# Kernel optimization log

Measured on AMD Instinct MI355X. Metric: run time of the kernel, lower is better.

## Reference

```python
import jax, jax.numpy as jnp
import numpy as np

DIM = 1024
HEADS = 16


def setup_inputs() -> dict:
    key = jax.random.key(0)
    ks = jax.random.split(key, 5)
    x = jax.random.normal(ks[0], (2, 2048, DIM), dtype=jnp.float32)
    # nn.Linear init-like scaling
    qkv_w = jax.random.normal(ks[1], (3 * DIM, DIM), dtype=jnp.float32) * (1.0 / np.sqrt(DIM))
    qkv_b = jax.random.normal(ks[2], (3 * DIM,), dtype=jnp.float32) * 0.02
    proj_w = jax.random.normal(ks[3], (DIM, DIM), dtype=jnp.float32) * (1.0 / np.sqrt(DIM))
    proj_b = jax.random.normal(ks[4], (DIM,), dtype=jnp.float32) * 0.02
    return {"x": x, "qkv_w": qkv_w, "qkv_b": qkv_b, "proj_w": proj_w, "proj_b": proj_b}


def reference(x, qkv_w, qkv_b, proj_w, proj_b):
    B, N, C = x.shape
    H = HEADS
    Dh = C // H
    scale = Dh ** -0.5
    # qkv: [B, N, 3C] -> [3, B, H, N, Dh]
    qkv = (x @ qkv_w.T + qkv_b).reshape(B, N, 3, H, Dh).transpose(2, 0, 3, 1, 4)
    q, k, v = qkv[0], qkv[1], qkv[2]
    attn = jnp.einsum('bhnd,bhmd->bhnm', q, k) * scale
    attn = jax.nn.softmax(attn, axis=-1)
    out = jnp.einsum('bhnm,bhmd->bhnd', attn, v)  # [B, H, N, Dh]
    out = out.transpose(0, 2, 1, 3).reshape(B, N, C)
    return out @ proj_w.T + proj_b
```

## Files before the change

### kernel.cpp

```cpp
#include <hip/hip_runtime.h>
#include <stdint.h>

#define DIM    1024
#define NHEADS 16
#define DH     64
#define SEQ    2048
#define BATCH  2
#define BHEADS (BATCH * NHEADS)
#define MROWS  (BATCH * SEQ)
#define SL2E   0.18033688011112042f

typedef __attribute__((ext_vector_type(8))) short bf16x8;
typedef __attribute__((ext_vector_type(4))) float f32x4;
typedef __attribute__((ext_vector_type(16))) float f32x16;
typedef unsigned short ushort_t;

#define GLDS(gp, lp) __builtin_amdgcn_global_load_lds( \
    (__attribute__((address_space(1))) void*)(gp), \
    (__attribute__((address_space(3))) void*)(lp), 16, 0, 0)

__device__ inline ushort_t f2bf(float f) {
    unsigned u = __builtin_bit_cast(unsigned, f);
    u += 0x7FFFu + ((u >> 16) & 1u);
    return (ushort_t)(u >> 16);
}

__global__ __launch_bounds__(256) void cvt_kernel(
    const float* __restrict__ s0, const float* __restrict__ s1, const float* __restrict__ s2,
    ushort_t* __restrict__ d0, ushort_t* __restrict__ d1, ushort_t* __restrict__ d2)
{
    const int N0 = MROWS * DIM;
    const int N1 = 3 * DIM * DIM;
    const int N2 = DIM * DIM;
    int e = (blockIdx.x * 256 + threadIdx.x) << 2;
    const float* src; ushort_t* dst;
    if (e < N0)                { src = s0 + e;             dst = d0 + e; }
    else if (e < N0 + N1)      { src = s1 + (e - N0);      dst = d1 + (e - N0); }
    else if (e < N0 + N1 + N2) { src = s2 + (e - N0 - N1); dst = d2 + (e - N0 - N1); }
    else return;
    float4 f = *(const float4*)src;
    ushort4 o;
    o.x = f2bf(f.x); o.y = f2bf(f.y); o.z = f2bf(f.z); o.w = f2bf(f.w);
    *(ushort4*)dst = o;
}

__global__ __launch_bounds__(512, 4) void qkv_gemm(
    const ushort_t* __restrict__ A, const ushort_t* __restrict__ W,
    const float* __restrict__ bias,
    ushort_t* __restrict__ Qw, ushort_t* __restrict__ Kw, ushort_t* __restrict__ Vt)
{
    __shared__ union {
        ushort_t stage[2][2][128 * 64];
        ushort_t T[128 * 136];
    } sm;

    const int tid  = threadIdx.x;
    const int lane = tid & 63;
    const int wave = tid >> 6;
    const int quad = lane >> 4;
    const int l16  = lane & 15;
    const int wm   = (wave >> 1) * 32;
    const int wn   = (wave & 1) * 64;
    const int bm   = blockIdx.x * 128;
    const int bn   = blockIdx.y * 128;
    const int Rl   = lane >> 3;
    const int pp   = lane & 7;

    f32x4 acc[2][4];
    for (int i = 0; i < 2; i++)
        for (int j = 0; j < 4; j++)
            for (int r = 0; r < 4; r++) acc[i][j][r] = 0.f;

    for (int j = 0; j < 2; j++) {
        int Rb = j * 64 + wave * 8;
        int R  = Rb + Rl;
        int c  = pp ^ (R & 7);
        GLDS(A + (size_t)(bm + R) * DIM + c * 8, sm.stage[0][0] + Rb * 64 + lane * 8);
        GLDS(W + (size_t)(bn + R) * DIM + c * 8, sm.stage[0][1] + Rb * 64 + lane * 8);
    }

    const int NT = DIM / 64;
    for (int t = 0; t < NT; t++) {
        if (t < NT - 1) {
            int kk = (t + 1) * 64;
            ushort_t* As1 = sm.stage[(t + 1) & 1][0];
            ushort_t* Bs1 = sm.stage[(t + 1) & 1][1];
            for (int j = 0; j < 2; j++) {
                int Rb = j * 64 + wave * 8;
                int R  = Rb + Rl;
                int c  = pp ^ (R & 7);
                GLDS(A + (size_t)(bm + R) * DIM + kk + c * 8, As1 + Rb * 64 + lane * 8);
                GLDS(W + (size_t)(bn + R) * DIM + kk + c * 8, Bs1 + Rb * 64 + lane * 8);
            }
            __asm volatile("s_waitcnt vmcnt(4)" ::: "memory");
        } else {
            __asm volatile("s_waitcnt vmcnt(0)" ::: "memory");
        }
        __asm volatile("s_barrier" ::: "memory");

        const ushort_t* Asb = sm.stage[t & 1][0];
        const ushort_t* Bsb = sm.stage[t & 1][1];
        for (int kh = 0; kh < 2; kh++) {
            bf16x8 a[2], b[4];
            for (int mi = 0; mi < 2; mi++) {
                int r = wm + mi * 16 + l16;
                a[mi] = *(const bf16x8*)(Asb + r * 64 + (((kh * 4 + quad) ^ (r & 7)) << 3));
            }
            for (int ni = 0; ni < 4; ni++) {
                int r = wn + ni * 16 + l16;
                b[ni] = *(const bf16x8*)(Bsb + r * 64 + (((kh * 4 + quad) ^ (r & 7)) << 3));
            }
            for (int mi = 0; mi < 2; mi++)
                for (int ni = 0; ni < 4; ni++)
                    acc[mi][ni] = __builtin_amdgcn_mfma_f32_16x16x32_bf16(a[mi], b[ni], acc[mi][ni], 0, 0, 0);
        }
        __asm volatile("s_waitcnt lgkmcnt(0)" ::: "memory");
        __asm volatile("s_barrier" ::: "memory");
    }

    const int three = bn >> 10;
    const float scale = (three == 0) ? SL2E : 1.0f;
    for (int ni = 0; ni < 4; ni++) {
        int cl   = wn + ni * 16 + l16;
        float bv = bias[bn + cl];
        for (int mi = 0; mi < 2; mi++)
            for (int reg = 0; reg < 4; reg++) {
                int r = wm + mi * 16 + quad * 4 + reg;
                sm.T[r * 136 + cl] = f2bf((acc[mi][ni][reg] + bv) * scale);
            }
    }
    __syncthreads();

    const int b = bm >> 11, npos0 = bm & 2047;
    if (three < 2) {
        int item = tid >> 1, sub = tid & 1;
        int r = item >> 1, hh = item & 1;
        int hc = (bn + hh * 64) & 1023;
        int h  = hc >> 6;
        ushort_t* dst = (three == 0 ? Qw : Kw) + ((size_t)(b * NHEADS + h) * SEQ + npos0 + r) * DH;
        const ushort_t* srcp = sm.T + r * 136 + hh * 64;
        for (int s = sub * 4; s < sub * 4 + 4; s++)
            *(uint4*)(dst + s * 8) = *(const uint4*)(srcp + s * 8);
    } else {
        int c = tid & 127, hh = (tid >> 7) & 1, sub = tid >> 8;
        int hc = (bn + c) & 1023;
        int h  = hc >> 6, d = hc & 63;
        ushort_t* dst = Vt + ((size_t)(b * NHEADS + h) * DH + d) * SEQ + npos0 + hh * 64;
        for (int s = sub * 4; s < sub * 4 + 4; s++) {
            union { ushort_t u[8]; uint4 v; } tmp;
            for (int k2 = 0; k2 < 8; k2++) {
                int o  = hh * 64 + s * 8 + k2;
                int po = (o & ~12) | ((o & 4) << 1) | ((o & 8) >> 1);
                tmp.u[k2] = sm.T[po * 136 + c];
            }
            *(uint4*)(dst + s * 8) = tmp.v;
        }
    }
}

__global__ __launch_bounds__(512, 4) void attn_kernel(
    const ushort_t* __restrict__ Qw, const ushort_t* __restrict__ Kw,
    const ushort_t* __restrict__ Vt, ushort_t* __restrict__ Ao)
{
    __shared__ union {
        ushort_t u[24576];
        float Lb[128][66];
    } sh;

    const int tid  = threadIdx.x;
    const int lane = tid & 63;
    const int wave = tid >> 6;
    const int grp  = wave >> 2;
    const int wg   = wave & 3;
    const int hi   = lane >> 5;
    const int l32  = lane & 31;
    const int Rl   = lane >> 3;
    const int pp   = lane & 7;

    const int bid  = blockIdx.x + 16 * blockIdx.y;
    const int bid2 = (bid & 7) * 64 + (bid >> 3);
    const int bh   = bid2 >> 4;
    const int q0   = (bid2 & 15) * 128;

    const ushort_t* Qh = Qw + (size_t)bh * SEQ * DH;
    const ushort_t* Kh = Kw + (size_t)bh * SEQ * DH;
    const ushort_t* Vh = Vt + (size_t)bh * DH * SEQ;

    ushort_t* const Qs = sh.u + 16384;

    for (int j = 0; j < 2; j++) {
        int Rb = j * 64 + wave * 8;
        int R  = Rb + Rl;
        int c  = pp ^ (R & 7);
        GLDS(Qh + (size_t)(q0 + R) * DH + c * 8, Qs + Rb * 64 + lane * 8);
    }
    for (int t = 0; t < 2; t++) {
        int R = wg * 8 + Rl;
        int c = pp ^ (R & 7);
        GLDS(Kh + (size_t)(t * 64 + grp * 32 + R) * DH + c * 8,
             sh.u + (t << 13) + grp * 2048 + wg * 512 + lane * 8);
        int Rd = wave * 8 + Rl;
        int cv = pp ^ (Rd & 7);
        GLDS(Vh + (size_t)Rd * SEQ + t * 64 + cv * 8,
             sh.u + (t << 13) + 4096 + wave * 512 + lane * 8);
    }
    __asm volatile("s_waitcnt vmcnt(2)" ::: "memory");
    __asm volatile("s_barrier" ::: "memory");

    bf16x8 qf[4];
    {
        int qr = wg * 32 + l32;
#pragma unroll
        for (int kt = 0; kt < 4; kt++)
            qf[kt] = *(const bf16x8*)(Qs + qr * 64 + (((2 * kt + hi) ^ (qr & 7)) << 3));
    }
    __asm volatile("s_waitcnt lgkmcnt(0)" ::: "memory");

    f32x16 oacc[2], liD, SZERO;
#pragma unroll
    for (int i = 0; i < 16; i++) { oacc[0][i] = 0.f; oacc[1][i] = 0.f; liD[i] = 0.f; SZERO[i] = 0.f; }
    bf16x8 vones;
#pragma unroll
    for (int i = 0; i < 8; i++) vones[i] = (short)0x3F80;

    const int NIT = 32;
    int cur = 0;
    for (int it = 0; it < NIT; it++) {
        if (it >= 1 && it < NIT - 1) {
            int nb = cur + 1; if (nb == 3) nb = 0;
            int kb = (it + 1) * 64;
            int R  = wg * 8 + Rl;
            int c  = pp ^ (R & 7);
            GLDS(Kh + (size_t)(kb + grp * 32 + R) * DH + c * 8,
                 sh.u + (nb << 13) + grp * 2048 + wg * 512 + lane * 8);
            int Rd = wave * 8 + Rl;
            int cv = pp ^ (Rd & 7);
            GLDS(Vh + (size_t)Rd * SEQ + kb + cv * 8,
                 sh.u + (nb << 13) + 4096 + wave * 512 + lane * 8);
        }
        if (it < NIT - 1) {
            __asm volatile("s_waitcnt vmcnt(2)" ::: "memory");
        } else {
            __asm volatile("s_waitcnt vmcnt(0)" ::: "memory");
        }
        __asm volatile("s_barrier" ::: "memory");

        const ushort_t* Ksb = sh.u + (cur << 13) + grp * 2048;
        const ushort_t* Vsb = sh.u + (cur << 13) + 4096;

        f32x16 S;
        __builtin_amdgcn_s_setprio(1);
#pragma unroll
        for (int kt = 0; kt < 4; kt++) {
            bf16x8 kf = *(const bf16x8*)(Ksb + l32 * 64 + (((2 * kt + hi) ^ (l32 & 7)) << 3));
            S = __builtin_amdgcn_mfma_f32_32x32x16_bf16(kf, qf[kt], kt == 0 ? SZERO : S, 0, 0, 0);
        }
        __builtin_amdgcn_s_setprio(0);

        unsigned Dw[8];
#pragma unroll
        for (int m = 0; m < 8; m++) {
            float p0 = __builtin_amdgcn_exp2f(S[2 * m]);
            float p1 = __builtin_amdgcn_exp2f(S[2 * m + 1]);
            unsigned d;
            asm("v_cvt_pk_bf16_f32 %0, %1, %2" : "=v"(d) : "v"(p0), "v"(p1));
            Dw[m] = d;
        }
        union { unsigned u[4]; bf16x8 v; } pc0, pc1;
        pc0.u[0] = Dw[0]; pc0.u[1] = Dw[1]; pc0.u[2] = Dw[2]; pc0.u[3] = Dw[3];
        pc1.u[0] = Dw[4]; pc1.u[1] = Dw[5]; pc1.u[2] = Dw[6]; pc1.u[3] = Dw[7];
        bf16x8 pa[2] = { pc0.v, pc1.v };

        __builtin_amdgcn_s_setprio(1);
        liD = __builtin_amdgcn_mfma_f32_32x32x16_bf16(pa[0], vones, liD, 0, 0, 0);
        liD = __builtin_amdgcn_mfma_f32_32x32x16_bf16(pa[1], vones, liD, 0, 0, 0);
#pragma unroll
        for (int kt = 0; kt < 2; kt++)
#pragma unroll
            for (int dh = 0; dh < 2; dh++) {
                int dr = dh * 32 + l32;
                bf16x8 vf = *(const bf16x8*)(Vsb + dr * 64 + (((grp * 4 + 2 * kt + hi) ^ (dr & 7)) << 3));
                oacc[dh] = __builtin_amdgcn_mfma_f32_32x32x16_bf16(pa[kt], vf, oacc[dh], 0, 0, 0);
            }
        __builtin_amdgcn_s_setprio(0);

        cur++; if (cur == 3) cur = 0;
    }

    __syncthreads();

    const int b = bh >> 4, h = bh & 15;
    if (grp == 1) {
#pragma unroll
        for (int dh = 0; dh < 2; dh++)
#pragma unroll
            for (int reg = 0; reg < 16; reg++) {
                int row = wg * 32 + (reg & 3) + 8 * (reg >> 2) + 4 * hi;
                sh.Lb[row][dh * 32 + l32] = oacc[dh][reg];
            }
        if (l32 == 0) {
#pragma unroll
            for (int reg = 0; reg < 16; reg++) {
                int row = wg * 32 + (reg & 3) + 8 * (reg >> 2) + 4 * hi;
                sh.Lb[row][64] = liD[reg];
            }
        }
    }
    __syncthreads();
    if (grp == 0) {
#pragma unroll
        for (int reg = 0; reg < 16; reg++) {
            int row = wg * 32 + (reg & 3) + 8 * (reg >> 2) + 4 * hi;
            float inv = 1.0f / (liD[reg] + sh.Lb[row][64]);
            int grow = q0 + row;
#pragma unroll
            for (int dh = 0; dh < 2; dh++) {
                float o = oacc[dh][reg] + sh.Lb[row][dh * 32 + l32];
                Ao[((size_t)b * SEQ + grow) * DIM + h * 64 + dh * 32 + l32] = f2bf(o * inv);
            }
        }
    }
}

__global__ __launch_bounds__(256, 4) void proj_gemm(
    const ushort_t* __restrict__ A, const ushort_t* __restrict__ W,
    const float* __restrict__ bias, float* __restrict__ Cout)
{
    __shared__ ushort_t Asd[2][128 * 64];
    __shared__ ushort_t Bsd[2][64 * 64];

    const int tid  = threadIdx.x;
    const int lane = tid & 63;
    const int wave = tid >> 6;
    const int quad = lane >> 4;
    const int l16  = lane & 15;
    const int wm   = (wave >> 1) * 64;
    const int wn   = (wave & 1) * 32;
    const int bm   = blockIdx.x * 128;
    const int bn   = blockIdx.y * 64;
    const int Rl   = lane >> 3;
    const int pp   = lane & 7;

    f32x4 acc[4][2];
    for (int i = 0; i < 4; i++)
        for (int j = 0; j < 2; j++)
            for (int r = 0; r < 4; r++) acc[i][j][r] = 0.f;

    for (int j = 0; j < 4; j++) {
        int Rb = j * 32 + wave * 8;
        int R  = Rb + Rl;
        int c  = pp ^ (R & 7);
        GLDS(A + (size_t)(bm + R) * DIM + c * 8, Asd[0] + Rb * 64 + lane * 8);
    }
    for (int j = 0; j < 2; j++) {
        int Rb = j * 32 + wave * 8;
        int R  = Rb + Rl;
        int c  = pp ^ (R & 7);
        GLDS(W + (size_t)(bn + R) * DIM + c * 8, Bsd[0] + Rb * 64 + lane * 8);
    }

    const int NT = DIM / 64;
    for (int t = 0; t < NT; t++) {
        if (t < NT - 1) {
            int kk = (t + 1) * 64;
            ushort_t* As1 = Asd[(t + 1) & 1];
            ushort_t* Bs1 = Bsd[(t + 1) & 1];
            for (int j = 0; j < 4; j++) {
                int Rb = j * 32 + wave * 8;
                int R  = Rb + Rl;
                int c  = pp ^ (R & 7);
                GLDS(A + (size_t)(bm + R) * DIM + kk + c * 8, As1 + Rb * 64 + lane * 8);
            }
            for (int j = 0; j < 2; j++) {
                int Rb = j * 32 + wave * 8;
                int R  = Rb + Rl;
                int c  = pp ^ (R & 7);
                GLDS(W + (size_t)(bn + R) * DIM + kk + c * 8, Bs1 + Rb * 64 + lane * 8);
            }
            __asm volatile("s_waitcnt vmcnt(6)" ::: "memory");
        } else {
            __asm volatile("s_waitcnt vmcnt(0)" ::: "memory");
        }
        __asm volatile("s_barrier" ::: "memory");

        const ushort_t* Asb = Asd[t & 1];
        const ushort_t* Bsb = Bsd[t & 1];
        for (int kh = 0; kh < 2; kh++) {
            bf16x8 a[4], b[2];
            for (int mi = 0; mi < 4; mi++) {
                int r = wm + mi * 16 + l16;
                a[mi] = *(const bf16x8*)(Asb + r * 64 + (((kh * 4 + quad) ^ (r & 7)) << 3));
            }
            for (int ni = 0; ni < 2; ni++) {
                int r = wn + ni * 16 + l16;
                b[ni] = *(const bf16x8*)(Bsb + r * 64 + (((kh * 4 + quad) ^ (r & 7)) << 3));
            }
            for (int mi = 0; mi < 4; mi++)
                for (int ni = 0; ni < 2; ni++)
                    acc[mi][ni] = __builtin_amdgcn_mfma_f32_16x16x32_bf16(a[mi], b[ni], acc[mi][ni], 0, 0, 0);
        }
        __asm volatile("s_waitcnt lgkmcnt(0)" ::: "memory");
        __asm volatile("s_barrier" ::: "memory");
    }

    for (int mi = 0; mi < 4; mi++) {
        for (int ni = 0; ni < 2; ni++) {
            int col  = bn + wn + ni * 16 + l16;
            float bv = bias[col];
            for (int reg = 0; reg < 4; reg++) {
                int row = bm + wm + mi * 16 + quad * 4 + reg;
                Cout[(size_t)row * DIM + col] = acc[mi][ni][reg] + bv;
            }
        }
    }
}

extern "C" void kernel_launch(void* const* d_in, const int* in_sizes, int n_in,
                              void* d_out, int out_size, void* d_ws, size_t ws_size,
                              hipStream_t stream) {
    const float* x      = (const float*)d_in[0];
    const float* qkv_w  = (const float*)d_in[1];
    const float* qkv_b  = (const float*)d_in[2];
    const float* proj_w = (const float*)d_in[3];
    const float* proj_b = (const float*)d_in[4];
    float* out = (float*)d_out;

    ushort_t* xb      = (ushort_t*)d_ws;
    ushort_t* qkv_wb  = xb      + (size_t)MROWS * DIM;
    ushort_t* proj_wb = qkv_wb  + (size_t)3 * DIM * DIM;
    ushort_t* Qw      = proj_wb + (size_t)DIM * DIM;
    ushort_t* Kw      = Qw      + (size_t)BHEADS * SEQ * DH;
    ushort_t* Vt      = Kw      + (size_t)BHEADS * SEQ * DH;
    ushort_t* Ao      = Vt      + (size_t)BHEADS * SEQ * DH;

    const int total_cvt = MROWS * DIM + 3 * DIM * DIM + DIM * DIM;
    cvt_kernel<<<total_cvt / (4 * 256), 256, 0, stream>>>(x, qkv_w, proj_w, xb, qkv_wb, proj_wb);
    qkv_gemm<<<dim3(MROWS / 128, (3 * DIM) / 128), 512, 0, stream>>>(xb, qkv_wb, qkv_b, Qw, Kw, Vt);
    attn_kernel<<<dim3(SEQ / 128, BHEADS), 512, 0, stream>>>(Qw, Kw, Vt, Ao);
    proj_gemm<<<dim3(MROWS / 128, DIM / 64), 256, 0, stream>>>(Ao, proj_wb, proj_b, out);
}
```

Measured before the change: 173.9 us.

## Remap GEMM blocks per XCD for L2 locality and widen proj_gemm to 512 threads

Both GEMMs now launch as a 1D grid, and the block index is remapped so that each of the 8 XCDs handles a contiguous 2D patch of output tiles (round-robin dispatch assumed). The goal is better L2 reuse of A and W tiles within each XCD. proj_gemm also moves from 4 to 8 waves, so each wave computes a 32x32 sub-tile instead of 64x32 and each thread issues fewer loads. This raises wave-level parallelism but lowers per-wave MFMA work relative to LDS reads, and the remap relies on dispatch order.

```diff
diff --git a/kernel.cpp b/kernel.cpp
--- a/kernel.cpp
+++ b/kernel.cpp
@@ -61,8 +61,13 @@
     const int l16  = lane & 15;
     const int wm   = (wave >> 1) * 32;
     const int wn   = (wave & 1) * 64;
-    const int bm   = blockIdx.x * 128;
-    const int bn   = blockIdx.y * 128;
+    const int bid  = blockIdx.x;
+    const int xcd  = bid & 7;
+    const int lidx = bid >> 3;
+    const int bx   = (xcd & 3) * 8 + (lidx & 7);
+    const int by   = (xcd >> 2) * 12 + (lidx >> 3);
+    const int bm   = bx * 128;
+    const int bn   = by * 128;
     const int Rl   = lane >> 3;
     const int pp   = lane & 7;
 
@@ -322,7 +327,7 @@
     }
 }
 
-__global__ __launch_bounds__(256, 4) void proj_gemm(
+__global__ __launch_bounds__(512, 4) void proj_gemm(
     const ushort_t* __restrict__ A, const ushort_t* __restrict__ W,
     const float* __restrict__ bias, float* __restrict__ Cout)
 {
@@ -334,29 +339,33 @@
     const int wave = tid >> 6;
     const int quad = lane >> 4;
     const int l16  = lane & 15;
-    const int wm   = (wave >> 1) * 64;
+    const int wm   = (wave >> 1) * 32;
     const int wn   = (wave & 1) * 32;
-    const int bm   = blockIdx.x * 128;
-    const int bn   = blockIdx.y * 64;
+    const int bid  = blockIdx.x;
+    const int xcd  = bid & 7;
+    const int lidx = bid >> 3;
+    const int bx   = (xcd & 3) * 8 + (lidx & 7);
+    const int by   = (xcd >> 2) * 8 + (lidx >> 3);
+    const int bm   = bx * 128;
+    const int bn   = by * 64;
     const int Rl   = lane >> 3;
     const int pp   = lane & 7;
 
-    f32x4 acc[4][2];
-    for (int i = 0; i < 4; i++)
+    f32x4 acc[2][2];
+    for (int i = 0; i < 2; i++)
         for (int j = 0; j < 2; j++)
             for (int r = 0; r < 4; r++) acc[i][j][r] = 0.f;
 
-    for (int j = 0; j < 4; j++) {
-        int Rb = j * 32 + wave * 8;
+    for (int j = 0; j < 2; j++) {
+        int Rb = j * 64 + wave * 8;
         int R  = Rb + Rl;
         int c  = pp ^ (R & 7);
         GLDS(A + (size_t)(bm + R) * DIM + c * 8, Asd[0] + Rb * 64 + lane * 8);
     }
-    for (int j = 0; j < 2; j++) {
-        int Rb = j * 32 + wave * 8;
-        int R  = Rb + Rl;
-        int c  = pp ^ (R & 7);
-        GLDS(W + (size_t)(bn + R) * DIM + c * 8, Bsd[0] + Rb * 64 + lane * 8);
+    {
+        int R = wave * 8 + Rl;
+        int c = pp ^ (R & 7);
+        GLDS(W + (size_t)(bn + R) * DIM + c * 8, Bsd[0] + wave * 512 + lane * 8);
     }
 
     const int NT = DIM / 64;
@@ -365,19 +374,18 @@
             int kk = (t + 1) * 64;
             ushort_t* As1 = Asd[(t + 1) & 1];
             ushort_t* Bs1 = Bsd[(t + 1) & 1];
-            for (int j = 0; j < 4; j++) {
-                int Rb = j * 32 + wave * 8;
+            for (int j = 0; j < 2; j++) {
+                int Rb = j * 64 + wave * 8;
                 int R  = Rb + Rl;
                 int c  = pp ^ (R & 7);
                 GLDS(A + (size_t)(bm + R) * DIM + kk + c * 8, As1 + Rb * 64 + lane * 8);
             }
-            for (int j = 0; j < 2; j++) {
-                int Rb = j * 32 + wave * 8;
-                int R  = Rb + Rl;
-                int c  = pp ^ (R & 7);
-                GLDS(W + (size_t)(bn + R) * DIM + kk + c * 8, Bs1 + Rb * 64 + lane * 8);
-            }
-            __asm volatile("s_waitcnt vmcnt(6)" ::: "memory");
+            {
+                int R = wave * 8 + Rl;
+                int c = pp ^ (R & 7);
+                GLDS(W + (size_t)(bn + R) * DIM + kk + c * 8, Bs1 + wave * 512 + lane * 8);
+            }
+            __asm volatile("s_waitcnt vmcnt(3)" ::: "memory");
         } else {
             __asm volatile("s_waitcnt vmcnt(0)" ::: "memory");
         }
@@ -386,8 +394,8 @@
         const ushort_t* Asb = Asd[t & 1];
         const ushort_t* Bsb = Bsd[t & 1];
         for (int kh = 0; kh < 2; kh++) {
-            bf16x8 a[4], b[2];
-            for (int mi = 0; mi < 4; mi++) {
+            bf16x8 a[2], b[2];
+            for (int mi = 0; mi < 2; mi++) {
                 int r = wm + mi * 16 + l16;
                 a[mi] = *(const bf16x8*)(Asb + r * 64 + (((kh * 4 + quad) ^ (r & 7)) << 3));
             }
@@ -395,7 +403,7 @@
                 int r = wn + ni * 16 + l16;
                 b[ni] = *(const bf16x8*)(Bsb + r * 64 + (((kh * 4 + quad) ^ (r & 7)) << 3));
             }
-            for (int mi = 0; mi < 4; mi++)
+            for (int mi = 0; mi < 2; mi++)
                 for (int ni = 0; ni < 2; ni++)
                     acc[mi][ni] = __builtin_amdgcn_mfma_f32_16x16x32_bf16(a[mi], b[ni], acc[mi][ni], 0, 0, 0);
         }
@@ -403,7 +411,7 @@
         __asm volatile("s_barrier" ::: "memory");
     }
 
-    for (int mi = 0; mi < 4; mi++) {
+    for (int mi = 0; mi < 2; mi++) {
         for (int ni = 0; ni < 2; ni++) {
             int col  = bn + wn + ni * 16 + l16;
             float bv = bias[col];
@@ -435,7 +443,7 @@
 
     const int total_cvt = MROWS * DIM + 3 * DIM * DIM + DIM * DIM;
     cvt_kernel<<<total_cvt / (4 * 256), 256, 0, stream>>>(x, qkv_w, proj_w, xb, qkv_wb, proj_wb);
-    qkv_gemm<<<dim3(MROWS / 128, (3 * DIM) / 128), 512, 0, stream>>>(xb, qkv_wb, qkv_b, Qw, Kw, Vt);
+    qkv_gemm<<<768, 512, 0, stream>>>(xb, qkv_wb, qkv_b, Qw, Kw, Vt);
     attn_kernel<<<dim3(SEQ / 128, BHEADS), 512, 0, stream>>>(Qw, Kw, Vt, Ao);
-    proj_gemm<<<dim3(MROWS / 128, DIM / 64), 256, 0, stream>>>(Ao, proj_wb, proj_b, out);
-}
+    proj_gemm<<<512, 512, 0, stream>>>(Ao, proj_wb, proj_b, out);
+}
```

Measured after the change: 174.1 us. Within noise of the previous version (+0.1%).
